# Optimization experiments

Hardware: AMD Instinct MI355X
Metric: run time of the kernel (lower is better)

## Reference

```python
import jax, jax.numpy as jnp
import numpy as np

N_NODES = 100000


def setup_inputs() -> dict:
    key = jax.random.key(0)
    k1, k2, k3 = jax.random.split(key, 3)
    x = jax.random.normal(k1, (100000, 64), dtype=jnp.float32)
    edge_index = jax.random.randint(k2, (2, 1000000), 0, 100000, dtype=jnp.int64)
    edge_attr = jax.random.uniform(k3, (1000000, 64), dtype=jnp.float32)
    return {"x": x, "edge_index": edge_index, "edge_attr": edge_attr}


def reference(x, edge_index, edge_attr):
    # gather source node features [E, d], weight by edge_attr, scatter-add to dest
    msg = x[edge_index[1]] * edge_attr  # [E, d]
    out = jax.ops.segment_sum(msg, edge_index[0], num_segments=N_NODES)  # [N, d]
    return out
```

## Files before the change

### kernel.cpp

```cpp
#include <hip/hip_runtime.h>
#include <hip/hip_bf16.h>


typedef float vfloat4 __attribute__((ext_vector_type(4)));

__global__ void scatter_mul_atomic(const float* __restrict__ x,
                                   const int* __restrict__ edge_index,
                                   const float* __restrict__ edge_attr,
                                   float* __restrict__ out,
                                   int E, int epw) {
    const int lane = threadIdx.x & 63;
    const int w = blockIdx.x * (blockDim.x >> 6) + (threadIdx.x >> 6);
    int e = w * epw;
    int e1 = e + epw;
    if (e1 > E) e1 = E;

    for (; e + 3 < e1; e += 4) {
        int d0 = edge_index[e],     d1 = edge_index[e + 1];
        int d2 = edge_index[e + 2], d3 = edge_index[e + 3];
        int s0 = edge_index[E + e],     s1 = edge_index[E + e + 1];
        int s2 = edge_index[E + e + 2], s3 = edge_index[E + e + 3];
        float a0 = __builtin_nontemporal_load(edge_attr + (size_t)e * 64 + lane);
        float a1 = __builtin_nontemporal_load(edge_attr + (size_t)(e + 1) * 64 + lane);
        float a2 = __builtin_nontemporal_load(edge_attr + (size_t)(e + 2) * 64 + lane);
        float a3 = __builtin_nontemporal_load(edge_attr + (size_t)(e + 3) * 64 + lane);
        float v0 = x[(size_t)s0 * 64 + lane];
        float v1 = x[(size_t)s1 * 64 + lane];
        float v2 = x[(size_t)s2 * 64 + lane];
        float v3 = x[(size_t)s3 * 64 + lane];
        atomicAdd(out + (size_t)d0 * 64 + lane, a0 * v0);
        atomicAdd(out + (size_t)d1 * 64 + lane, a1 * v1);
        atomicAdd(out + (size_t)d2 * 64 + lane, a2 * v2);
        atomicAdd(out + (size_t)d3 * 64 + lane, a3 * v3);
    }
    for (; e < e1; e++) {
        int d = edge_index[e], s = edge_index[E + e];
        float a = __builtin_nontemporal_load(edge_attr + (size_t)e * 64 + lane);
        atomicAdd(out + (size_t)d * 64 + lane, a * x[(size_t)s * 64 + lane]);
    }
}

extern "C" void kernel_launch(void* const* d_in, const int* in_sizes, int n_in,
                              void* d_out, int out_size, void* d_ws, size_t ws_size,
                              hipStream_t stream) {
    const float* x          = (const float*)d_in[0];
    const int*   edge_index = (const int*)d_in[1];
    const float* edge_attr  = (const float*)d_in[2];
    float*       out        = (float*)d_out;

    const int E = in_sizes[1] / 2;

    hipMemsetAsync(out, 0, (size_t)out_size * sizeof(float), stream);

    const int block = 256;
    const int grid = 2048;
    const int waves = grid * (block / 64);
    const int epw = (E + waves - 1) / waves;
    scatter_mul_atomic<<<grid, block, 0, stream>>>(x, edge_index, edge_attr,
                                                   out, E, epw);
}
```

Measured before the change: 507.1 us.

## Partition destination nodes across block teams to localize atomic scatter traffic

Blocks are split into eight teams, each owning one contiguous eighth of the destination node range. Every team scans all edges, loading indices one per lane, and uses a ballot to keep only edges whose destination lies in its range; those edges are then processed with shuffled indices. The intent is to concentrate each team's atomics on a smaller slice of the output, on the assumption that interleaved block IDs map to distinct XCDs and their L2 caches, which would improve atomic locality. In exchange, every edge index is read eight times and per-wave work becomes serialized and irregular.

```diff
diff --git a/kernel.cpp b/kernel.cpp
--- a/kernel.cpp
+++ b/kernel.cpp
@@ -4,39 +4,43 @@
 
 typedef float vfloat4 __attribute__((ext_vector_type(4)));
 
-__global__ void scatter_mul_atomic(const float* __restrict__ x,
-                                   const int* __restrict__ edge_index,
-                                   const float* __restrict__ edge_attr,
-                                   float* __restrict__ out,
-                                   int E, int epw) {
+#define NTEAMS 8
+
+__global__ void scatter_part_kernel(const float* __restrict__ x,
+                                    const int* __restrict__ edge_index,
+                                    const float* __restrict__ edge_attr,
+                                    float* __restrict__ out,
+                                    int E, int N, int epw) {
     const int lane = threadIdx.x & 63;
-    const int w = blockIdx.x * (blockDim.x >> 6) + (threadIdx.x >> 6);
-    int e = w * epw;
-    int e1 = e + epw;
+    const int r = blockIdx.x & (NTEAMS - 1);
+    const int wv = (blockIdx.x >> 3) * (blockDim.x >> 6) + (threadIdx.x >> 6);
+    const int rlo = (int)(((long long)N * r) >> 3);
+    const int rhi = (int)(((long long)N * (r + 1)) >> 3);
+
+    int e0 = wv * epw;
+    int e1 = e0 + epw;
     if (e1 > E) e1 = E;
 
-    for (; e + 3 < e1; e += 4) {
-        int d0 = edge_index[e],     d1 = edge_index[e + 1];
-        int d2 = edge_index[e + 2], d3 = edge_index[e + 3];
-        int s0 = edge_index[E + e],     s1 = edge_index[E + e + 1];
-        int s2 = edge_index[E + e + 2], s3 = edge_index[E + e + 3];
-        float a0 = __builtin_nontemporal_load(edge_attr + (size_t)e * 64 + lane);
-        float a1 = __builtin_nontemporal_load(edge_attr + (size_t)(e + 1) * 64 + lane);
-        float a2 = __builtin_nontemporal_load(edge_attr + (size_t)(e + 2) * 64 + lane);
-        float a3 = __builtin_nontemporal_load(edge_attr + (size_t)(e + 3) * 64 + lane);
-        float v0 = x[(size_t)s0 * 64 + lane];
-        float v1 = x[(size_t)s1 * 64 + lane];
-        float v2 = x[(size_t)s2 * 64 + lane];
-        float v3 = x[(size_t)s3 * 64 + lane];
-        atomicAdd(out + (size_t)d0 * 64 + lane, a0 * v0);
-        atomicAdd(out + (size_t)d1 * 64 + lane, a1 * v1);
-        atomicAdd(out + (size_t)d2 * 64 + lane, a2 * v2);
-        atomicAdd(out + (size_t)d3 * 64 + lane, a3 * v3);
-    }
-    for (; e < e1; e++) {
-        int d = edge_index[e], s = edge_index[E + e];
-        float a = __builtin_nontemporal_load(edge_attr + (size_t)e * 64 + lane);
-        atomicAdd(out + (size_t)d * 64 + lane, a * x[(size_t)s * 64 + lane]);
+    for (int b = e0; b < e1; b += 64) {
+        const int e = b + lane;
+        int d = -1, s = 0;
+        if (e < e1) {
+            d = edge_index[e];
+            s = edge_index[E + e];
+        }
+        const bool ok = (d >= rlo) && (d < rhi);
+        unsigned long long m = __ballot(ok);
+        while (m) {
+            const int bit = __ffsll((long long)m) - 1;
+            m &= m - 1;
+            const int ee = b + bit;
+            const int dd = __shfl(d, bit, 64);
+            const int ss = __shfl(s, bit, 64);
+            const float a = __builtin_nontemporal_load(
+                edge_attr + (size_t)ee * 64 + lane);
+            const float v = x[(size_t)ss * 64 + lane];
+            atomicAdd(out + (size_t)dd * 64 + lane, a * v);
+        }
     }
 }
 
@@ -49,13 +53,14 @@
     float*       out        = (float*)d_out;
 
     const int E = in_sizes[1] / 2;
+    const int N = out_size / 64;
 
     hipMemsetAsync(out, 0, (size_t)out_size * sizeof(float), stream);
 
     const int block = 256;
     const int grid = 2048;
-    const int waves = grid * (block / 64);
-    const int epw = (E + waves - 1) / waves;
-    scatter_mul_atomic<<<grid, block, 0, stream>>>(x, edge_index, edge_attr,
-                                                   out, E, epw);
+    const int waves_per_team = (grid / NTEAMS) * (block / 64);
+    const int epw = (E + waves_per_team - 1) / waves_per_team;
+    scatter_part_kernel<<<grid, block, 0, stream>>>(x, edge_index, edge_attr,
+                                                    out, E, N, epw);
 }
```

Measured after the change: 529.5 us. 1.04x slower.
